# Kernel tuning notes

Hardware: AMD Instinct MI355X
Metric: run time of the kernel (lower is better)

Reference implementation:

```python
import jax, jax.numpy as jnp
import numpy as np

N, E, B, STEPS, THETAS, F, R = 20000, 40000, 32, 32, 64, 3, 1.0


def setup_inputs() -> dict:
    key = jax.random.key(0)
    k1, k2, k3, k4 = jax.random.split(key, 4)
    x = jax.random.normal(k1, (N, F), dtype=jnp.float32)
    v = jax.random.normal(k2, (F, THETAS), dtype=jnp.float32)
    v = v / jnp.linalg.norm(v, axis=0, keepdims=True)  # sphere constraint on directions
    lin = jnp.linspace(-R, R, STEPS, dtype=jnp.float32)
    edge_index = jax.random.randint(k3, (2, E), 0, N, dtype=jnp.int64)
    batch = jnp.sort(jax.random.randint(k4, (N,), 0, B, dtype=jnp.int64))
    return {"x": x, "v": v, "lin": lin, "edge_index": edge_index, "batch": batch}


def _ecc(h, idx, lin, num_segments):
    # h: [M, T] heights; idx: [M] graph ids; lin: [S] thresholds
    # sigmoid(200*(lin - h)) -> [M, S, T], then segment-sum over M -> [B, S, T]
    e = jax.nn.sigmoid(200.0 * (lin[None, :, None] - h[:, None, :]))
    return jax.ops.segment_sum(e, idx, num_segments=num_segments)


def reference(x, v, lin, edge_index, batch):
    nh = x @ v                                            # [N, T] node heights
    eh = jnp.maximum(nh[edge_index[0]], nh[edge_index[1]])  # [E, T] edge heights (max of endpoints)
    edge_batch = batch[edge_index[0]]                     # [E]
    ect_nodes = _ecc(nh, batch, lin, B)                   # [B, S, T]
    ect_edges = _ecc(eh, edge_batch, lin, B)              # [B, S, T]
    return ect_nodes - ect_edges / 2
```

## Files before the change

kernel.cpp:

```cpp
#include <hip/hip_runtime.h>

#define N_NODES 20000
#define N_EDGES 40000
#define NB 32
#define NS 32
#define NT 64
#define EPC 1024
#define NCH 40
#define NPREP 64
#define CAP 2048
#define KBN 8
#define KBE 16
#define STEP200 12.9032258065f
#define WB 0.992f


__global__ __launch_bounds__(256) void prep_kernel(
        const int* __restrict__ ei, const int* __restrict__ batch,
        int* __restrict__ ecnt, int* __restrict__ node_base,
        int2* __restrict__ sedge, float* __restrict__ out_zero) {
    const int t = threadIdx.x;
    const int bid = blockIdx.x;
    for (int idx = bid * 256 + t; idx < NB * NS * NT; idx += NPREP * 256)
        out_zero[idx] = 0.0f;

    if (bid < NCH) {
        __shared__ int h[NB];
        __shared__ int basep[NB];
        int bb[4], ss[4], dd[4];
        if (t < NB) h[t] = 0;
        __syncthreads();
#pragma unroll
        for (int k = 0; k < 4; k++) {
            const int e = bid * EPC + k * 256 + t;
            bb[k] = -1;
            if (e < N_EDGES) {
                ss[k] = ei[e];
                dd[k] = ei[N_EDGES + e];
                bb[k] = batch[ss[k]];
                atomicAdd(&h[bb[k]], 1);
            }
        }
        __syncthreads();
        if (t < NB) {
            basep[t] = atomicAdd(&ecnt[t], h[t]);
            h[t] = 0;
        }
        __syncthreads();
#pragma unroll
        for (int k = 0; k < 4; k++) {
            if (bb[k] >= 0) {
                const int p = atomicAdd(&h[bb[k]], 1);
                const int g = basep[bb[k]] + p;
                if (g < CAP) sedge[bb[k] * CAP + g] = make_int2(ss[k], dd[k]);
            }
        }
    } else if (bid < 60) {
#pragma unroll
        for (int k = 0; k < 4; k++) {
            const int n = (bid - NCH) * 1024 + k * 256 + t;
            if (n < N_NODES) {
                const int bn = batch[n];
                const int bp = (n == 0) ? -1 : batch[n - 1];
                for (int q = bp + 1; q <= bn; q++) node_base[q] = n;
                if (n == N_NODES - 1)
                    for (int q = bn + 1; q <= NB; q++) node_base[q] = N_NODES;
            }
        }
    }
}

__global__ __launch_bounds__(256) void ect_main_kernel(
        const float* __restrict__ x, const float* __restrict__ v,
        const int* __restrict__ node_base, const int* __restrict__ ecnt,
        const int2* __restrict__ sedge,
        float* __restrict__ out) {
    __shared__ float acc[NS * NT];
    __shared__ int diff[(NS + 1) * NT];
    const int t = threadIdx.x;
#pragma unroll
    for (int j = 0; j < 8; j++) acc[t + 256 * j] = 0.0f;
    for (int idx = t; idx < (NS + 1) * NT; idx += 256) diff[idx] = 0;
    __syncthreads();

    const int lane = t & 63;
    const int wid = __builtin_amdgcn_readfirstlane(t >> 6);
    const bool is_node = blockIdx.x < NB * KBN;
    int b, hi, i0, stride; float w;
    if (is_node) {
        b = blockIdx.x / KBN;
        const int slice = blockIdx.x % KBN;
        const int lo = node_base[b]; hi = node_base[b + 1];
        i0 = lo + slice * 4 + wid; stride = KBN * 4; w = 1.0f;
    } else {
        const int q = blockIdx.x - NB * KBN;
        b = q / KBE;
        const int slice = q % KBE;
        const int lo = b * CAP; hi = lo + ecnt[b];
        i0 = lo + slice * 4 + wid; stride = KBE * 4; w = -0.5f;
    }
    const float v0 = v[lane], v1 = v[NT + lane], v2 = v[2 * NT + lane];

    if (is_node) {
        for (int i = i0; i < hi; i += stride) {
            const float h = fmaf(x[3 * i], v0, fmaf(x[3 * i + 1], v1, x[3 * i + 2] * v2));
            const float t200h = 200.0f * h;
            const float u = (h + 1.0f) * 15.5f;
            const int kb = (int)ceilf(u - WB);
            const int ke = (int)floorf(u + WB) + 1;
#pragma unroll
            for (int j = 0; j < 2; j++) {
                const int s = kb + j;
                if (s < ke && s >= 0 && s < NS) {
                    const float z = fmaf((float)s, STEP200, -200.0f) - t200h;
                    const float sig = __builtin_amdgcn_rcpf(1.0f + __expf(-z));
                    atomicAdd(&acc[s * NT + lane], sig);
                }
            }
            const int kec = min(max(ke, 0), NS);
            atomicAdd(&diff[kec * NT + lane], 1);
        }
    } else {
        int i = i0;
        if (i < hi) {
            int2 e2 = sedge[i];
            while (i < hi) {
                const int inext = i + stride;
                const int2 cur = e2;
                if (inext < hi) e2 = sedge[inext];
                const float hs = fmaf(x[3 * cur.x], v0, fmaf(x[3 * cur.x + 1], v1, x[3 * cur.x + 2] * v2));
                const float hd = fmaf(x[3 * cur.y], v0, fmaf(x[3 * cur.y + 1], v1, x[3 * cur.y + 2] * v2));
                const float h = fmaxf(hs, hd);
                const float t200h = 200.0f * h;
                const float u = (h + 1.0f) * 15.5f;
                const int kb = (int)ceilf(u - WB);
                const int ke = (int)floorf(u + WB) + 1;
#pragma unroll
                for (int j = 0; j < 2; j++) {
                    const int s = kb + j;
                    if (s < ke && s >= 0 && s < NS) {
                        const float z = fmaf((float)s, STEP200, -200.0f) - t200h;
                        const float sig = __builtin_amdgcn_rcpf(1.0f + __expf(-z));
                        atomicAdd(&acc[s * NT + lane], sig);
                    }
                }
                const int kec = min(max(ke, 0), NS);
                atomicAdd(&diff[kec * NT + lane], 1);
                i = inext;
            }
        }
    }
    __syncthreads();

    if (t < NT) {
        int run = 0;
#pragma unroll
        for (int s = 0; s < NS; s++) {
            run += diff[s * NT + t];
            acc[s * NT + t] += (float)run;
        }
    }
    __syncthreads();

    float* ob = out + b * (NS * NT);
#pragma unroll
    for (int j = 0; j < 8; j++) {
        const int idx = t + 256 * j;
        const float val = acc[idx];
        if (val != 0.0f) atomicAdd(&ob[idx], w * val);
    }
}

extern "C" void kernel_launch(void* const* d_in, const int* in_sizes, int n_in,
                              void* d_out, int out_size, void* d_ws, size_t ws_size,
                              hipStream_t stream) {
    const float* x   = (const float*)d_in[0];
    const float* v   = (const float*)d_in[1];
    const int*   ei  = (const int*)d_in[3];
    const int*   bat = (const int*)d_in[4];

    float* out = (float*)d_out;

    int* ecnt      = (int*)d_ws;
    int* node_base = ecnt + NB;
    int2* sedge    = (int2*)((int*)d_ws + 72);

    hipMemsetAsync(ecnt, 0, NB * sizeof(int), stream);
    prep_kernel<<<NPREP, 256, 0, stream>>>(ei, bat, ecnt, node_base, sedge, out);
    ect_main_kernel<<<NB * (KBN + KBE), 256, 0, stream>>>(
        x, v, node_base, ecnt, sedge, out);
}
```

Baseline: 97.53 us.

## Pre-gather edge endpoint coordinates in prep and batch loads in main loop

Result: slower. 117.6 us (+20.6%).

```diff
diff --git a/kernel.cpp b/kernel.cpp
--- a/kernel.cpp
+++ b/kernel.cpp
@@ -5,60 +5,77 @@
 #define NB 32
 #define NS 32
 #define NT 64
-#define EPC 1024
-#define NCH 40
-#define NPREP 64
-#define CAP 2048
+#define NSC 160
+#define NPREP 192
+#define CAPB 1536
 #define KBN 8
 #define KBE 16
 #define STEP200 12.9032258065f
 #define WB 0.992f
 
 
+__device__ __forceinline__ void accum_item(float h, int lane,
+                                           float* __restrict__ acc,
+                                           float* __restrict__ fdiff) {
+    const float t200h = 200.0f * h;
+    const float u = (h + 1.0f) * 15.5f;
+    const int kb = (int)ceilf(u - WB);
+    const int ke = (int)floorf(u + WB) + 1;
+#pragma unroll
+    for (int j = 0; j < 2; j++) {
+        const int s = kb + j;
+        if (s < ke && s >= 0 && s < NS) {
+            const float z = fmaf((float)s, STEP200, -200.0f) - t200h;
+            const float sig = __builtin_amdgcn_rcpf(1.0f + __expf(-z));
+            atomicAdd(&acc[s * NT + lane], sig);
+        }
+    }
+    const int kec = min(max(ke, 0), NS);
+    atomicAdd(&fdiff[kec * NT + lane], 1.0f);
+}
+
 __global__ __launch_bounds__(256) void prep_kernel(
-        const int* __restrict__ ei, const int* __restrict__ batch,
-        int* __restrict__ ecnt, int* __restrict__ node_base,
-        int2* __restrict__ sedge, float* __restrict__ out_zero) {
+        const float* __restrict__ x, const int* __restrict__ ei,
+        const int* __restrict__ batch, int* __restrict__ ecnt,
+        int* __restrict__ node_base, float4* __restrict__ sedge,
+        float* __restrict__ out_zero) {
     const int t = threadIdx.x;
     const int bid = blockIdx.x;
     for (int idx = bid * 256 + t; idx < NB * NS * NT; idx += NPREP * 256)
         out_zero[idx] = 0.0f;
 
-    if (bid < NCH) {
+    if (bid < NSC) {
         __shared__ int h[NB];
         __shared__ int basep[NB];
-        int bb[4], ss[4], dd[4];
         if (t < NB) h[t] = 0;
         __syncthreads();
-#pragma unroll
-        for (int k = 0; k < 4; k++) {
-            const int e = bid * EPC + k * 256 + t;
-            bb[k] = -1;
-            if (e < N_EDGES) {
-                ss[k] = ei[e];
-                dd[k] = ei[N_EDGES + e];
-                bb[k] = batch[ss[k]];
-                atomicAdd(&h[bb[k]], 1);
-            }
+        const int e = bid * 256 + t;
+        int b = -1, s = 0, d = 0;
+        if (e < N_EDGES) {
+            s = ei[e];
+            d = ei[N_EDGES + e];
+            b = batch[s];
+            atomicAdd(&h[b], 1);
         }
         __syncthreads();
-        if (t < NB) {
+        if (t < NB && h[t] > 0) {
             basep[t] = atomicAdd(&ecnt[t], h[t]);
             h[t] = 0;
         }
         __syncthreads();
+        if (b >= 0) {
+            const int p = atomicAdd(&h[b], 1);
+            const int g = basep[b] + p;
+            if (g < CAPB) {
+                float4* ep = sedge + (size_t)(b * CAPB + g) * 2;
+                ep[0] = make_float4(x[3 * s], x[3 * s + 1], x[3 * s + 2], x[3 * d]);
+                ep[1] = make_float4(x[3 * d + 1], x[3 * d + 2], 0.0f, 0.0f);
+            }
+        }
+    } else if (bid < NSC + 20) {
 #pragma unroll
         for (int k = 0; k < 4; k++) {
-            if (bb[k] >= 0) {
-                const int p = atomicAdd(&h[bb[k]], 1);
-                const int g = basep[bb[k]] + p;
-                if (g < CAP) sedge[bb[k] * CAP + g] = make_int2(ss[k], dd[k]);
-            }
-        }
-    } else if (bid < 60) {
-#pragma unroll
-        for (int k = 0; k < 4; k++) {
-            const int n = (bid - NCH) * 1024 + k * 256 + t;
+            const int n = (bid - NSC) * 1024 + k * 256 + t;
             if (n < N_NODES) {
                 const int bn = batch[n];
                 const int bp = (n == 0) ? -1 : batch[n - 1];
@@ -73,95 +90,82 @@
 __global__ __launch_bounds__(256) void ect_main_kernel(
         const float* __restrict__ x, const float* __restrict__ v,
         const int* __restrict__ node_base, const int* __restrict__ ecnt,
-        const int2* __restrict__ sedge,
-        float* __restrict__ out) {
+        const float4* __restrict__ sedge, float* __restrict__ out) {
     __shared__ float acc[NS * NT];
-    __shared__ int diff[(NS + 1) * NT];
+    __shared__ float fdiff[(NS + 1) * NT];
     const int t = threadIdx.x;
 #pragma unroll
     for (int j = 0; j < 8; j++) acc[t + 256 * j] = 0.0f;
-    for (int idx = t; idx < (NS + 1) * NT; idx += 256) diff[idx] = 0;
+    for (int idx = t; idx < (NS + 1) * NT; idx += 256) fdiff[idx] = 0.0f;
     __syncthreads();
 
     const int lane = t & 63;
     const int wid = __builtin_amdgcn_readfirstlane(t >> 6);
     const bool is_node = blockIdx.x < NB * KBN;
-    int b, hi, i0, stride; float w;
+    const float v0 = v[lane], v1 = v[NT + lane], v2 = v[2 * NT + lane];
+    int b;
+
     if (is_node) {
         b = blockIdx.x / KBN;
         const int slice = blockIdx.x % KBN;
-        const int lo = node_base[b]; hi = node_base[b + 1];
-        i0 = lo + slice * 4 + wid; stride = KBN * 4; w = 1.0f;
+        const int lo = node_base[b], hi = node_base[b + 1];
+        const int i0 = lo + slice * 4 + wid;
+        for (int base = i0; base < hi; base += 4 * 32) {
+            float ax[4], ay[4], az[4];
+#pragma unroll
+            for (int k = 0; k < 4; k++) {
+                const int i = base + k * 32;
+                if (i < hi) { ax[k] = x[3 * i]; ay[k] = x[3 * i + 1]; az[k] = x[3 * i + 2]; }
+            }
+#pragma unroll
+            for (int k = 0; k < 4; k++) {
+                const int i = base + k * 32;
+                if (i < hi)
+                    accum_item(fmaf(ax[k], v0, fmaf(ay[k], v1, az[k] * v2)),
+                               lane, acc, fdiff);
+            }
+        }
     } else {
         const int q = blockIdx.x - NB * KBN;
         b = q / KBE;
         const int slice = q % KBE;
-        const int lo = b * CAP; hi = lo + ecnt[b];
-        i0 = lo + slice * 4 + wid; stride = KBE * 4; w = -0.5f;
-    }
-    const float v0 = v[lane], v1 = v[NT + lane], v2 = v[2 * NT + lane];
-
-    if (is_node) {
-        for (int i = i0; i < hi; i += stride) {
-            const float h = fmaf(x[3 * i], v0, fmaf(x[3 * i + 1], v1, x[3 * i + 2] * v2));
-            const float t200h = 200.0f * h;
-            const float u = (h + 1.0f) * 15.5f;
-            const int kb = (int)ceilf(u - WB);
-            const int ke = (int)floorf(u + WB) + 1;
+        const int lo = b * CAPB;
+        const int hi = lo + min(ecnt[b], CAPB);
+        const int i0 = lo + slice * 4 + wid;
+        for (int base = i0; base < hi; base += 4 * 64) {
+            float4 A[4], B[4];
 #pragma unroll
-            for (int j = 0; j < 2; j++) {
-                const int s = kb + j;
-                if (s < ke && s >= 0 && s < NS) {
-                    const float z = fmaf((float)s, STEP200, -200.0f) - t200h;
-                    const float sig = __builtin_amdgcn_rcpf(1.0f + __expf(-z));
-                    atomicAdd(&acc[s * NT + lane], sig);
+            for (int k = 0; k < 4; k++) {
+                const int i = base + k * 64;
+                if (i < hi) {
+                    const float4* ep = sedge + (size_t)i * 2;
+                    A[k] = ep[0]; B[k] = ep[1];
                 }
             }
-            const int kec = min(max(ke, 0), NS);
-            atomicAdd(&diff[kec * NT + lane], 1);
-        }
-    } else {
-        int i = i0;
-        if (i < hi) {
-            int2 e2 = sedge[i];
-            while (i < hi) {
-                const int inext = i + stride;
-                const int2 cur = e2;
-                if (inext < hi) e2 = sedge[inext];
-                const float hs = fmaf(x[3 * cur.x], v0, fmaf(x[3 * cur.x + 1], v1, x[3 * cur.x + 2] * v2));
-                const float hd = fmaf(x[3 * cur.y], v0, fmaf(x[3 * cur.y + 1], v1, x[3 * cur.y + 2] * v2));
-                const float h = fmaxf(hs, hd);
-                const float t200h = 200.0f * h;
-                const float u = (h + 1.0f) * 15.5f;
-                const int kb = (int)ceilf(u - WB);
-                const int ke = (int)floorf(u + WB) + 1;
 #pragma unroll
-                for (int j = 0; j < 2; j++) {
-                    const int s = kb + j;
-                    if (s < ke && s >= 0 && s < NS) {
-                        const float z = fmaf((float)s, STEP200, -200.0f) - t200h;
-                        const float sig = __builtin_amdgcn_rcpf(1.0f + __expf(-z));
-                        atomicAdd(&acc[s * NT + lane], sig);
-                    }
+            for (int k = 0; k < 4; k++) {
+                const int i = base + k * 64;
+                if (i < hi) {
+                    const float hs = fmaf(A[k].x, v0, fmaf(A[k].y, v1, A[k].z * v2));
+                    const float hd = fmaf(A[k].w, v0, fmaf(B[k].x, v1, B[k].y * v2));
+                    accum_item(fmaxf(hs, hd), lane, acc, fdiff);
                 }
-                const int kec = min(max(ke, 0), NS);
-                atomicAdd(&diff[kec * NT + lane], 1);
-                i = inext;
             }
         }
     }
     __syncthreads();
 
     if (t < NT) {
-        int run = 0;
+        float run = 0.0f;
 #pragma unroll
         for (int s = 0; s < NS; s++) {
-            run += diff[s * NT + t];
-            acc[s * NT + t] += (float)run;
+            run += fdiff[s * NT + t];
+            acc[s * NT + t] += run;
         }
     }
     __syncthreads();
 
+    const float w = is_node ? 1.0f : -0.5f;
     float* ob = out + b * (NS * NT);
 #pragma unroll
     for (int j = 0; j < 8; j++) {
@@ -183,10 +187,10 @@
 
     int* ecnt      = (int*)d_ws;
     int* node_base = ecnt + NB;
-    int2* sedge    = (int2*)((int*)d_ws + 72);
+    float4* sedge  = (float4*)((int*)d_ws + 72);
 
     hipMemsetAsync(ecnt, 0, NB * sizeof(int), stream);
-    prep_kernel<<<NPREP, 256, 0, stream>>>(ei, bat, ecnt, node_base, sedge, out);
+    prep_kernel<<<NPREP, 256, 0, stream>>>(x, ei, bat, ecnt, node_base, sedge, out);
     ect_main_kernel<<<NB * (KBN + KBE), 256, 0, stream>>>(
         x, v, node_base, ecnt, sedge, out);
 }
```
